# Performance work log

Measured on AMD Instinct MI355X. Metric: run time of the kernel, lower is better.

The kernel has to match this reference:

```python
import jax, jax.numpy as jnp
import numpy as np

N = 100000   # nodes
E = 1600000  # edges
C = 128      # d_model
F = 6        # LIFT_FEATURES
L = 2        # num_gcn_layers
EPS = 1e-5

def _gelu(v):
    return jax.nn.gelu(v, approximate=False)  # torch nn.GELU() default = exact erf

def setup_inputs() -> dict:
    key = jax.random.key(0)
    ks = jax.random.split(key, 24)
    def w(k, shape):
        fan_in = shape[-2] if len(shape) >= 2 else shape[-1]
        return (jax.random.normal(k, shape, jnp.float32) / np.sqrt(fan_in)).astype(jnp.float32)
    inp = {
        "x": jax.random.normal(ks[0], (1, N, 9), jnp.float32),
        "edge_index": jax.random.randint(ks[1], (2, E), 0, N, jnp.int32),
        "edge_values": jax.random.uniform(ks[2], (E,), jnp.float32),
        # lift MLP
        "lift_w1": w(ks[3], (F, C)), "lift_b1": jnp.zeros((C,), jnp.float32),
        "lift_w2": w(ks[4], (C, C)), "lift_b2": jnp.zeros((C,), jnp.float32),
        # GCN layer params stacked over L layers
        "self_w": w(ks[5], (L, C, C)),  "self_b": jnp.zeros((L, C), jnp.float32),
        "neigh_w": w(ks[6], (L, C, C)), "neigh_b": jnp.zeros((L, C), jnp.float32),
        "gate_w1": w(ks[7], (L, 2 * C, C)), "gate_b1": jnp.zeros((L, C), jnp.float32),
        "gate_w2": w(ks[8], (L, C, C)),     "gate_b2": jnp.zeros((L, C), jnp.float32),
        # final LayerNorm
        "norm_g": jnp.ones((C,), jnp.float32), "norm_b": jnp.zeros((C,), jnp.float32),
    }
    return inp

def reference(x, edge_index, edge_values,
              lift_w1, lift_b1, lift_w2, lift_b2,
              self_w, self_b, neigh_w, neigh_b,
              gate_w1, gate_b1, gate_w2, gate_b2,
              norm_g, norm_b):
    # node_feats = x[..., 3:], B == 1 path -> work on [N, F]
    nf = x[0, :, 3:]
    h = _gelu(nf @ lift_w1 + lift_b1) @ lift_w2 + lift_b2  # [N, C]
    row, col = edge_index[0], edge_index[1]
    for l in range(L):
        neighbor = h @ neigh_w[l] + neigh_b[l]                 # [N, C]
        messages = neighbor[col] * edge_values[:, None]        # gather + weight [E, C]
        aggr = jnp.zeros_like(h).at[row].add(messages)         # scatter-add [N, C]
        self_f = h @ self_w[l] + self_b[l]                     # [N, C]
        u = jnp.concatenate([self_f, aggr], axis=-1)           # [N, 2C]
        u = _gelu(u @ gate_w1[l] + gate_b1[l]) @ gate_w2[l] + gate_b2[l]
        h = h + u
    mu = jnp.mean(h, axis=-1, keepdims=True)
    var = jnp.mean(jnp.square(h - mu), axis=-1, keepdims=True)
    h = (h - mu) * jax.lax.rsqrt(var + EPS) * norm_g + norm_b
    return h[None]  # [1, N, C]
```

## Files before the change

kernel.cpp:

```cpp
#include <hip/hip_runtime.h>
#include <math.h>

#define C 128

typedef unsigned short u16;
typedef __attribute__((ext_vector_type(8))) short short8;
typedef __attribute__((ext_vector_type(4))) float f32x4;

__device__ __forceinline__ float gelu_f(float v) {
    return 0.5f * v * (1.0f + erff(v * 0.70710678118654752f));
}

__device__ __forceinline__ u16 f2bf(float f) {
    unsigned u = __float_as_uint(f);
    unsigned r = (u + 0x7fffu + ((u >> 16) & 1u)) >> 16;
    return (u16)r;
}
__device__ __forceinline__ float b2f(u16 u) {
    return __uint_as_float(((unsigned)u) << 16);
}

__device__ __forceinline__ void g2lds16(const void* g, void* l) {
    __builtin_amdgcn_global_load_lds(
        (const __attribute__((address_space(1))) unsigned int*)g,
        (__attribute__((address_space(3))) unsigned int*)l, 16, 0, 0);
}

__global__ void prep_weights_kernel(const float* __restrict__ self_w,
                                    const float* __restrict__ self_b,
                                    const float* __restrict__ neigh_w,
                                    const float* __restrict__ neigh_b,
                                    const float* __restrict__ gate_w1,
                                    const float* __restrict__ gate_b1,
                                    float* __restrict__ Wc, float* __restrict__ bc,
                                    float* __restrict__ Wn1, float* __restrict__ bv,
                                    int L_) {
    const int y = blockIdx.y;
    const int i = blockIdx.x;
    const int j = threadIdx.x;
    if (y < L_) {
        const int l = y;
        const float* gw = gate_w1 + (size_t)l * 256 * C;
        if (i < C) {
            const float* swr = self_w + (size_t)l * C * C + (size_t)i * C;
            float s = 0.f;
            for (int k = 0; k < C; ++k) s += swr[k] * gw[k * C + j];
            Wc[(size_t)l * C * C + (size_t)i * C + j] = s;
        } else {
            const float* sbr = self_b + (size_t)l * C;
            float s = gate_b1[(size_t)l * C + j];
            for (int k = 0; k < C; ++k) s += sbr[k] * gw[k * C + j];
            bc[(size_t)l * C + j] = s;
        }
    } else {
        const int l = y - L_;
        const float* gw = gate_w1 + (size_t)l * 256 * C + (size_t)C * C;
        if (i < C) {
            const float* nwr = neigh_w + (size_t)l * C * C + (size_t)i * C;
            float s = 0.f;
            for (int k = 0; k < C; ++k) s += nwr[k] * gw[k * C + j];
            Wn1[(size_t)l * C * C + (size_t)i * C + j] = s;
        } else {
            const float* nbr = neigh_b + (size_t)l * C;
            float s = 0.f;
            for (int k = 0; k < C; ++k) s += nbr[k] * gw[k * C + j];
            bv[(size_t)l * C + j] = s;
        }
    }
}

__global__ void wsplit_kernel(const float* __restrict__ lw2, const float* __restrict__ gw2,
                              const float* __restrict__ Wc, const float* __restrict__ Wn1,
                              u16* __restrict__ wh, u16* __restrict__ wl) {
    const int col = blockIdx.x;
    const int mat = blockIdx.y;
    const int k = threadIdx.x;
    const float* src;
    if (mat == 0)      src = lw2;
    else if (mat <= 2) src = gw2 + (size_t)(mat - 1) * 16384;
    else if (mat <= 4) src = Wc + (size_t)(mat - 3) * 16384;
    else               src = Wn1 + (size_t)(mat - 5) * 16384;
    float v = src[k * C + col];
    u16 hi = f2bf(v);
    size_t di = (size_t)mat * 16384 + (size_t)col * C + k;
    wh[di] = hi;
    wl[di] = f2bf(v - b2f(hi));
}

__global__ void lift_hidden_kernel(const float* __restrict__ x,
                                   const float* __restrict__ w1,
                                   const float* __restrict__ b1,
                                   u16* __restrict__ oh, u16* __restrict__ ol, int N) {
    int idx = blockIdx.x * 256 + threadIdx.x;
    if (idx >= N * C) return;
    int n = idx >> 7, c = idx & 127;
    const float* xr = x + n * 9 + 3;
    float s = b1[c];
#pragma unroll
    for (int f = 0; f < 6; ++f) s += xr[f] * w1[f * C + c];
    s = gelu_f(s);
    u16 hi = f2bf(s);
    oh[idx] = hi;
    ol[idx] = f2bf(s - b2f(hi));
}

__global__ __launch_bounds__(256, 2)
void gemm_mfma_kernel(const u16* __restrict__ A0h, const u16* __restrict__ A0l,
                      const u16* __restrict__ W0h, const u16* __restrict__ W0l,
                      const u16* __restrict__ A1h, const u16* __restrict__ A1l,
                      const u16* __restrict__ W1h, const u16* __restrict__ W1l,
                      const float* __restrict__ bias,
                      const float* __restrict__ bias2,
                      const float* __restrict__ rowscale,
                      const u16* __restrict__ Rh, const u16* __restrict__ Rl,
                      u16* __restrict__ Oh, u16* __restrict__ Ol,
                      const float* __restrict__ lng, const float* __restrict__ lnb,
                      float* __restrict__ outF,
                      int M, int nsrc, int act) {
    __shared__ __align__(16) char smem[128 * 132 * 4];
    u16* lds0 = (u16*)smem;
    const int t = threadIdx.x;
    const int l = t & 63;
    const int w = t >> 6;
    const int wr = w >> 1, wc = w & 1;
    const int m0 = blockIdx.x * 128;
    const int kg = l >> 4;
    const int swz = l & 7;
    const int l15 = l & 15;

    f32x4 acc[4][4];
#pragma unroll
    for (int m = 0; m < 4; ++m)
#pragma unroll
        for (int n = 0; n < 4; ++n) acc[m][n] = (f32x4)(0.f);

    for (int sidx = 0; sidx < nsrc; ++sidx) {
        const u16* Ah = sidx ? A1h : A0h;
        const u16* Al = sidx ? A1l : A0l;
        const u16* Wh = sidx ? W1h : W0h;
        const u16* Wl = sidx ? W1l : W0l;
        for (int kh = 0; kh < 2; ++kh) {
            const u16* gp[4] = {Ah, Al, Wh, Wl};
#pragma unroll
            for (int p = 0; p < 4; ++p) {
#pragma unroll
                for (int it = 0; it < 4; ++it) {
                    int chunk = it * 256 + t;
                    int row = chunk >> 3;
                    int cl = (chunk & 7) ^ (row & 7);
                    int grow = (p < 2) ? ((m0 + row < M) ? m0 + row : M - 1) : row;
                    const u16* src = gp[p] + (size_t)grow * C + kh * 64 + cl * 8;
                    g2lds16(src, lds0 + (size_t)p * 8192 + chunk * 8);
                }
            }
            __syncthreads();
#pragma unroll
            for (int s = 0; s < 2; ++s) {
                const int ci = ((s * 4 + kg) ^ swz) * 16;
                short8 ah[4], al[4], bh[4], bl[4];
#pragma unroll
                for (int m = 0; m < 4; ++m) {
                    int ro = (wr * 64 + m * 16 + l15) * 128;
                    ah[m] = *(const short8*)((const char*)lds0 + ro + ci);
                    al[m] = *(const short8*)((const char*)lds0 + 16384 + ro + ci);
                }
#pragma unroll
                for (int n = 0; n < 4; ++n) {
                    int ro = (wc * 64 + n * 16 + l15) * 128;
                    bh[n] = *(const short8*)((const char*)lds0 + 32768 + ro + ci);
                    bl[n] = *(const short8*)((const char*)lds0 + 49152 + ro + ci);
                }
#pragma unroll
                for (int m = 0; m < 4; ++m)
#pragma unroll
                    for (int n = 0; n < 4; ++n)
                        acc[m][n] = __builtin_amdgcn_mfma_f32_16x16x32_bf16(ah[m], bh[n], acc[m][n], 0, 0, 0);
#pragma unroll
                for (int m = 0; m < 4; ++m)
#pragma unroll
                    for (int n = 0; n < 4; ++n)
                        acc[m][n] = __builtin_amdgcn_mfma_f32_16x16x32_bf16(al[m], bh[n], acc[m][n], 0, 0, 0);
#pragma unroll
                for (int m = 0; m < 4; ++m)
#pragma unroll
                    for (int n = 0; n < 4; ++n)
                        acc[m][n] = __builtin_amdgcn_mfma_f32_16x16x32_bf16(ah[m], bl[n], acc[m][n], 0, 0, 0);
            }
            __syncthreads();
        }
    }

    float* lnt = (float*)smem;
    float bj[4], b2j[4];
#pragma unroll
    for (int n = 0; n < 4; ++n) {
        bj[n] = bias[wc * 64 + n * 16 + l15];
        b2j[n] = bias2 ? bias2[wc * 64 + n * 16 + l15] : 0.f;
    }
#pragma unroll
    for (int m = 0; m < 4; ++m) {
#pragma unroll
        for (int r = 0; r < 4; ++r) {
            int rowl = wr * 64 + m * 16 + kg * 4 + r;
            int grow = m0 + rowl;
            bool ok = grow < M;
            float rs_ = (bias2 && ok) ? rowscale[grow] : 0.f;
#pragma unroll
            for (int n = 0; n < 4; ++n) {
                int col = wc * 64 + n * 16 + l15;
                float o = acc[m][n][r] + bj[n];
                if (bias2) o += rs_ * b2j[n];
                if (act) o = gelu_f(o);
                size_t idx = (size_t)grow * C + col;
                if (Rh && ok) o += b2f(Rh[idx]) + b2f(Rl[idx]);
                if (outF) {
                    lnt[rowl * 132 + col] = o;
                } else if (ok) {
                    u16 hi = f2bf(o);
                    Oh[idx] = hi;
                    Ol[idx] = f2bf(o - b2f(hi));
                }
            }
        }
    }

    if (outF) {
        __syncthreads();
        float2 gg = *(const float2*)&lng[l << 1];
        float2 bb = *(const float2*)&lnb[l << 1];
        for (int r = 0; r < 32; ++r) {
            int rowl = w * 32 + r;
            int grow = m0 + rowl;
            if (grow >= M) break;
            float2 v = *(const float2*)&lnt[rowl * 132 + (l << 1)];
            float s = v.x + v.y;
#pragma unroll
            for (int mk = 1; mk < 64; mk <<= 1) s += __shfl_xor(s, mk, 64);
            float mu = s * (1.f / 128.f);
            float dx = v.x - mu, dy = v.y - mu;
            float q = dx * dx + dy * dy;
#pragma unroll
            for (int mk = 1; mk < 64; mk <<= 1) q += __shfl_xor(q, mk, 64);
            float rsq = 1.f / sqrtf(q * (1.f / 128.f) + 1e-5f);
            float2 o;
            o.x = dx * rsq * gg.x + bb.x;
            o.y = dy * rsq * gg.y + bb.y;
            *(float2*)&outF[(size_t)grow * C + (l << 1)] = o;
        }
    }
}

__global__ void zero_i32_kernel(int* __restrict__ p, int n) {
    int i = blockIdx.x * 256 + threadIdx.x;
    if (i < n) p[i] = 0;
}

__global__ void deg_count_kernel(const int* __restrict__ row, int* __restrict__ deg, int E) {
    int e = blockIdx.x * 256 + threadIdx.x;
    if (e < E) atomicAdd(&deg[row[e]], 1);
}

__global__ void scan_chunk_kernel(const int* __restrict__ deg, int* __restrict__ offs,
                                  int* __restrict__ part, int N) {
    __shared__ int ts[256];
    const int t = threadIdx.x;
    const int base = blockIdx.x * 1024 + t * 4;
    int v0 = (base + 0 < N) ? deg[base + 0] : 0;
    int v1 = (base + 1 < N) ? deg[base + 1] : 0;
    int v2 = (base + 2 < N) ? deg[base + 2] : 0;
    int v3 = (base + 3 < N) ? deg[base + 3] : 0;
    int l0 = v0, l1 = l0 + v1, l2 = l1 + v2, l3 = l2 + v3;
    ts[t] = l3;
    __syncthreads();
    for (int d = 1; d < 256; d <<= 1) {
        int add = (t >= d) ? ts[t - d] : 0;
        __syncthreads();
        ts[t] += add;
        __syncthreads();
    }
    int tex = ts[t] - l3;
    if (base + 0 < N) offs[base + 1] = tex + l0;
    if (base + 1 < N) offs[base + 2] = tex + l1;
    if (base + 2 < N) offs[base + 3] = tex + l2;
    if (base + 3 < N) offs[base + 4] = tex + l3;
    if (t == 255) part[blockIdx.x] = ts[255];
}

__global__ void scan_partials_kernel(int* __restrict__ part, int n) {
    __shared__ int s[128];
    const int t = threadIdx.x;
    int v = (t < n) ? part[t] : 0;
    s[t] = v;
    __syncthreads();
    for (int d = 1; d < 128; d <<= 1) {
        int add = (t >= d) ? s[t - d] : 0;
        __syncthreads();
        s[t] += add;
        __syncthreads();
    }
    if (t < n) part[t] = s[t] - v;
}

__global__ void scan_add_kernel(int* __restrict__ offs, const int* __restrict__ part,
                                int* __restrict__ cursor, int N) {
    const int t = threadIdx.x;
    const int base = blockIdx.x * 1024 + t * 4;
    const int add = part[blockIdx.x];
#pragma unroll
    for (int j = 0; j < 4; ++j) {
        int i = base + j;
        if (i < N) {
            int v = offs[i + 1] + add;
            offs[i + 1] = v;
            if (i + 1 < N) cursor[i + 1] = v;
        }
    }
    if (blockIdx.x == 0 && t == 0) {
        offs[0] = 0;
        cursor[0] = 0;
    }
}

__global__ void fill_kernel(const int* __restrict__ row, const int* __restrict__ col,
                            const float* __restrict__ ev, int* __restrict__ cursor,
                            int2* __restrict__ epack, int E) {
    int e = blockIdx.x * 256 + threadIdx.x;
    if (e >= E) return;
    int r = row[e];
    int pos = atomicAdd(&cursor[r], 1);
    int2 p;
    p.x = col[e];
    p.y = __float_as_int(ev[e]);
    epack[pos] = p;
}

__global__ __launch_bounds__(256)
void aggregate_kernel(const u16* __restrict__ nh, const u16* __restrict__ nl,
                      const int* __restrict__ offs, const int2* __restrict__ epack,
                      u16* __restrict__ oh, u16* __restrict__ ol,
                      float* __restrict__ sumev, int N) {
    const int lane = threadIdx.x & 63;
    const int node = (blockIdx.x << 2) + (threadIdx.x >> 6);
    if (node >= N) return;
    const int s = offs[node], e = offs[node + 1];
    const int ch = lane << 1;
    float ax = 0.f, ay = 0.f, bx = 0.f, by = 0.f, ssum = 0.f;
    int i = s;
    for (; i + 2 <= e; i += 2) {
        int2 p0 = epack[i];
        int2 p1 = epack[i + 1];
        float v0 = __int_as_float(p0.y);
        float v1 = __int_as_float(p1.y);
        ushort2 h0 = *(const ushort2*)&nh[(size_t)p0.x * C + ch];
        ushort2 l0 = *(const ushort2*)&nl[(size_t)p0.x * C + ch];
        ushort2 h1 = *(const ushort2*)&nh[(size_t)p1.x * C + ch];
        ushort2 l1 = *(const ushort2*)&nl[(size_t)p1.x * C + ch];
        ax += v0 * (b2f(h0.x) + b2f(l0.x));
        ay += v0 * (b2f(h0.y) + b2f(l0.y));
        bx += v1 * (b2f(h1.x) + b2f(l1.x));
        by += v1 * (b2f(h1.y) + b2f(l1.y));
        ssum += v0 + v1;
    }
    if (i < e) {
        int2 p = epack[i];
        float v = __int_as_float(p.y);
        ushort2 h0 = *(const ushort2*)&nh[(size_t)p.x * C + ch];
        ushort2 l0 = *(const ushort2*)&nl[(size_t)p.x * C + ch];
        ax += v * (b2f(h0.x) + b2f(l0.x));
        ay += v * (b2f(h0.y) + b2f(l0.y));
        ssum += v;
    }
    float sx = ax + bx, sy = ay + by;
    ushort2 ho, lo;
    ho.x = f2bf(sx); ho.y = f2bf(sy);
    lo.x = f2bf(sx - b2f(ho.x)); lo.y = f2bf(sy - b2f(ho.y));
    size_t idx = (size_t)node * C + ch;
    *(ushort2*)&oh[idx] = ho;
    *(ushort2*)&ol[idx] = lo;
    if (lane == 0) sumev[node] = ssum;
}

extern "C" void kernel_launch(void* const* d_in, const int* in_sizes, int n_in,
                              void* d_out, int out_size, void* d_ws, size_t ws_size,
                              hipStream_t stream) {
    const float* x    = (const float*)d_in[0];
    const int*   ei   = (const int*)d_in[1];
    const float* ev   = (const float*)d_in[2];
    const float* lw1  = (const float*)d_in[3];
    const float* lb1  = (const float*)d_in[4];
    const float* lw2  = (const float*)d_in[5];
    const float* lb2  = (const float*)d_in[6];
    const float* sw   = (const float*)d_in[7];
    const float* sb   = (const float*)d_in[8];
    const float* nw   = (const float*)d_in[9];
    const float* nbi  = (const float*)d_in[10];
    const float* gw1  = (const float*)d_in[11];
    const float* gb1  = (const float*)d_in[12];
    const float* gw2  = (const float*)d_in[13];
    const float* gb2  = (const float*)d_in[14];
    const float* ng   = (const float*)d_in[15];
    const float* nbt  = (const float*)d_in[16];

    const int N = in_sizes[0] / 9;
    const int E = in_sizes[2];
    const int L = in_sizes[7] / (C * C);
    const int* row = ei;
    const int* col = ei + E;

    float* out = (float*)d_out;

    char* p = (char*)d_ws;
    u16* Hh = (u16*)p; p += (size_t)N * C * 2;
    u16* Hl = (u16*)p; p += (size_t)N * C * 2;
    u16* Bh = (u16*)p; p += (size_t)N * C * 2;
    u16* Bl = (u16*)p; p += (size_t)N * C * 2;
    u16* Ch = (u16*)p; p += (size_t)N * C * 2;
    u16* Cl = (u16*)p; p += (size_t)N * C * 2;
    int2* epack = (int2*)p; p += (size_t)E * sizeof(int2);
    float* Wc  = (float*)p; p += (size_t)L * C * C * sizeof(float);
    float* Wn1 = (float*)p; p += (size_t)L * C * C * sizeof(float);
    float* bc  = (float*)p; p += (size_t)L * C * sizeof(float);
    float* bv  = (float*)p; p += (size_t)L * C * sizeof(float);
    float* sumev = (float*)p; p += (size_t)N * sizeof(float);
    u16* wh = (u16*)p; p += (size_t)7 * C * C * 2;
    u16* wl = (u16*)p; p += (size_t)7 * C * C * 2;
    int* deg    = (int*)p; p += (size_t)N * sizeof(int);
    int* offs   = (int*)p; p += (size_t)(N + 1) * sizeof(int);
    int* cursor = (int*)p; p += (size_t)N * sizeof(int);
    int* part   = (int*)p; p += 1024 * sizeof(int);

    const int NB_SCAN = (N + 1023) / 1024;
    const int GB_NODE = (N + 3) / 4;
    const int GB_EDGE = (E + 255) / 256;
    const int GB_GEMM = (N + 127) / 128;

    prep_weights_kernel<<<dim3(C + 1, 2 * L), C, 0, stream>>>(
        sw, sb, nw, nbi, gw1, gb1, Wc, bc, Wn1, bv, L);
    wsplit_kernel<<<dim3(C, 7), C, 0, stream>>>(lw2, gw2, Wc, Wn1, wh, wl);

    lift_hidden_kernel<<<(N * C + 255) / 256, 256, 0, stream>>>(x, lw1, lb1, Bh, Bl, N);
    gemm_mfma_kernel<<<GB_GEMM, 256, 0, stream>>>(
        Bh, Bl, wh, wl, nullptr, nullptr, nullptr, nullptr,
        lb2, nullptr, nullptr, nullptr, nullptr, Hh, Hl,
        nullptr, nullptr, nullptr, N, 1, 0);

    zero_i32_kernel<<<(N + 255) / 256, 256, 0, stream>>>(deg, N);
    deg_count_kernel<<<GB_EDGE, 256, 0, stream>>>(row, deg, E);
    scan_chunk_kernel<<<NB_SCAN, 256, 0, stream>>>(deg, offs, part, N);
    scan_partials_kernel<<<1, 128, 0, stream>>>(part, NB_SCAN);
    scan_add_kernel<<<NB_SCAN, 256, 0, stream>>>(offs, part, cursor, N);
    fill_kernel<<<GB_EDGE, 256, 0, stream>>>(row, col, ev, cursor, epack, E);

    for (int l = 0; l < L; ++l) {
        const u16* g2h = wh + (size_t)(1 + l) * 16384;
        const u16* g2l = wl + (size_t)(1 + l) * 16384;
        const u16* wch = wh + (size_t)(3 + l) * 16384;
        const u16* wcl = wl + (size_t)(3 + l) * 16384;
        const u16* n1h = wh + (size_t)(5 + l) * 16384;
        const u16* n1l = wl + (size_t)(5 + l) * 16384;
        const bool last = (l == L - 1);

        aggregate_kernel<<<GB_NODE, 256, 0, stream>>>(Hh, Hl, offs, epack, Ch, Cl, sumev, N);
        gemm_mfma_kernel<<<GB_GEMM, 256, 0, stream>>>(
            Hh, Hl, wch, wcl, Ch, Cl, n1h, n1l,
            bc + (size_t)l * C, bv + (size_t)l * C, sumev,
            nullptr, nullptr, Bh, Bl,
            nullptr, nullptr, nullptr, N, 2, 1);
        gemm_mfma_kernel<<<GB_GEMM, 256, 0, stream>>>(
            Bh, Bl, g2h, g2l, nullptr, nullptr, nullptr, nullptr,
            gb2 + (size_t)l * C, nullptr, nullptr,
            Hh, Hl,
            last ? nullptr : Hh, last ? nullptr : Hl,
            last ? ng : nullptr, last ? nbt : nullptr, last ? out : nullptr,
            N, 1, 0);
    }
}
```

Measured before the change: 870.2 us.

## Fuse gate GEMMs into one layer kernel and unroll aggregation by four

Merges the concat GEMM with GELU and the second gate GEMM into one kernel. The GELU intermediate is written straight into LDS as hi/lo bf16 planes instead of round-tripping through global memory, and the residual add and LayerNorm epilogue are kept. The aggregation loop is unrolled to four edges with separate accumulators, which adds memory-level parallelism on the gathers. The fused kernel keeps a larger accumulator set live, so register pressure and occupancy could suffer.

```diff
diff --git a/kernel.cpp b/kernel.cpp
--- a/kernel.cpp
+++ b/kernel.cpp
@@ -104,21 +104,26 @@
     ol[idx] = f2bf(s - b2f(hi));
 }
 
+__device__ __forceinline__ void stage_plane(const u16* __restrict__ g, char* lds_base,
+                                            int p, int t, int kh, int m0, int M,
+                                            bool clampA) {
+#pragma unroll
+    for (int it = 0; it < 4; ++it) {
+        int chunk = it * 256 + t;
+        int row = chunk >> 3;
+        int cl = (chunk & 7) ^ (row & 7);
+        int grow = clampA ? ((m0 + row < M) ? m0 + row : M - 1) : row;
+        const u16* src = g + (size_t)grow * C + kh * 64 + cl * 8;
+        g2lds16(src, lds_base + (size_t)p * 16384 + chunk * 16);
+    }
+}
+
 __global__ __launch_bounds__(256, 2)
-void gemm_mfma_kernel(const u16* __restrict__ A0h, const u16* __restrict__ A0l,
-                      const u16* __restrict__ W0h, const u16* __restrict__ W0l,
-                      const u16* __restrict__ A1h, const u16* __restrict__ A1l,
-                      const u16* __restrict__ W1h, const u16* __restrict__ W1l,
+void gemm_mfma_kernel(const u16* __restrict__ Ah_, const u16* __restrict__ Al_,
+                      const u16* __restrict__ Wh_, const u16* __restrict__ Wl_,
                       const float* __restrict__ bias,
-                      const float* __restrict__ bias2,
-                      const float* __restrict__ rowscale,
-                      const u16* __restrict__ Rh, const u16* __restrict__ Rl,
-                      u16* __restrict__ Oh, u16* __restrict__ Ol,
-                      const float* __restrict__ lng, const float* __restrict__ lnb,
-                      float* __restrict__ outF,
-                      int M, int nsrc, int act) {
-    __shared__ __align__(16) char smem[128 * 132 * 4];
-    u16* lds0 = (u16*)smem;
+                      u16* __restrict__ Oh, u16* __restrict__ Ol, int M) {
+    __shared__ __align__(16) char smem[65536];
     const int t = threadIdx.x;
     const int l = t & 63;
     const int w = t >> 6;
@@ -134,25 +139,108 @@
 #pragma unroll
         for (int n = 0; n < 4; ++n) acc[m][n] = (f32x4)(0.f);
 
-    for (int sidx = 0; sidx < nsrc; ++sidx) {
-        const u16* Ah = sidx ? A1h : A0h;
-        const u16* Al = sidx ? A1l : A0l;
-        const u16* Wh = sidx ? W1h : W0h;
-        const u16* Wl = sidx ? W1l : W0l;
+    for (int kh = 0; kh < 2; ++kh) {
+        stage_plane(Ah_, smem, 0, t, kh, m0, M, true);
+        stage_plane(Al_, smem, 1, t, kh, m0, M, true);
+        stage_plane(Wh_, smem, 2, t, kh, m0, M, false);
+        stage_plane(Wl_, smem, 3, t, kh, m0, M, false);
+        __syncthreads();
+#pragma unroll
+        for (int s = 0; s < 2; ++s) {
+            const int ci = ((s * 4 + kg) ^ swz) * 16;
+            short8 ah[4], al[4], bh[4], bl[4];
+#pragma unroll
+            for (int m = 0; m < 4; ++m) {
+                int ro = (wr * 64 + m * 16 + l15) * 128;
+                ah[m] = *(const short8*)(smem + ro + ci);
+                al[m] = *(const short8*)(smem + 16384 + ro + ci);
+            }
+#pragma unroll
+            for (int n = 0; n < 4; ++n) {
+                int ro = (wc * 64 + n * 16 + l15) * 128;
+                bh[n] = *(const short8*)(smem + 32768 + ro + ci);
+                bl[n] = *(const short8*)(smem + 49152 + ro + ci);
+            }
+#pragma unroll
+            for (int m = 0; m < 4; ++m)
+#pragma unroll
+                for (int n = 0; n < 4; ++n)
+                    acc[m][n] = __builtin_amdgcn_mfma_f32_16x16x32_bf16(ah[m], bh[n], acc[m][n], 0, 0, 0);
+#pragma unroll
+            for (int m = 0; m < 4; ++m)
+#pragma unroll
+                for (int n = 0; n < 4; ++n)
+                    acc[m][n] = __builtin_amdgcn_mfma_f32_16x16x32_bf16(al[m], bh[n], acc[m][n], 0, 0, 0);
+#pragma unroll
+            for (int m = 0; m < 4; ++m)
+#pragma unroll
+                for (int n = 0; n < 4; ++n)
+                    acc[m][n] = __builtin_amdgcn_mfma_f32_16x16x32_bf16(ah[m], bl[n], acc[m][n], 0, 0, 0);
+        }
+        __syncthreads();
+    }
+
+    float bj[4];
+#pragma unroll
+    for (int n = 0; n < 4; ++n) bj[n] = bias[wc * 64 + n * 16 + l15];
+#pragma unroll
+    for (int m = 0; m < 4; ++m)
+#pragma unroll
+        for (int r = 0; r < 4; ++r) {
+            int grow = m0 + wr * 64 + m * 16 + kg * 4 + r;
+            if (grow < M) {
+#pragma unroll
+                for (int n = 0; n < 4; ++n) {
+                    int col = wc * 64 + n * 16 + l15;
+                    float o = acc[m][n][r] + bj[n];
+                    size_t idx = (size_t)grow * C + col;
+                    u16 hi = f2bf(o);
+                    Oh[idx] = hi;
+                    Ol[idx] = f2bf(o - b2f(hi));
+                }
+            }
+        }
+}
+
+__global__ __launch_bounds__(256, 2)
+void fused_layer_kernel(const u16* __restrict__ Hh, const u16* __restrict__ Hl,
+                        const u16* __restrict__ Chh, const u16* __restrict__ Cll,
+                        const u16* __restrict__ wch, const u16* __restrict__ wcl,
+                        const u16* __restrict__ n1h, const u16* __restrict__ n1l,
+                        const u16* __restrict__ g2h, const u16* __restrict__ g2l,
+                        const float* __restrict__ bc, const float* __restrict__ bv,
+                        const float* __restrict__ sumev,
+                        const float* __restrict__ gb2,
+                        u16* __restrict__ OHh, u16* __restrict__ OHl,
+                        const float* __restrict__ lng, const float* __restrict__ lnb,
+                        float* __restrict__ outF,
+                        int M) {
+    __shared__ __align__(16) char smem[128 * 132 * 4];
+    const int t = threadIdx.x;
+    const int l = t & 63;
+    const int w = t >> 6;
+    const int wr = w >> 1, wc = w & 1;
+    const int m0 = blockIdx.x * 128;
+    const int kg = l >> 4;
+    const int swz = l & 7;
+    const int l15 = l & 15;
+
+    f32x4 acc[4][4];
+#pragma unroll
+    for (int m = 0; m < 4; ++m)
+#pragma unroll
+        for (int n = 0; n < 4; ++n) acc[m][n] = (f32x4)(0.f);
+
+    for (int sidx = 0; sidx < 2; ++sidx) {
+        const u16* Ah_ = sidx ? Chh : Hh;
+        const u16* Al_ = sidx ? Cll : Hl;
+        const u16* Wh_ = sidx ? n1h : wch;
+        const u16* Wl_ = sidx ? n1l : wcl;
         for (int kh = 0; kh < 2; ++kh) {
-            const u16* gp[4] = {Ah, Al, Wh, Wl};
-#pragma unroll
-            for (int p = 0; p < 4; ++p) {
-#pragma unroll
-                for (int it = 0; it < 4; ++it) {
-                    int chunk = it * 256 + t;
-                    int row = chunk >> 3;
-                    int cl = (chunk & 7) ^ (row & 7);
-                    int grow = (p < 2) ? ((m0 + row < M) ? m0 + row : M - 1) : row;
-                    const u16* src = gp[p] + (size_t)grow * C + kh * 64 + cl * 8;
-                    g2lds16(src, lds0 + (size_t)p * 8192 + chunk * 8);
-                }
-            }
+            stage_plane(Ah_, smem, 0, t, kh, m0, M, true);
+            stage_plane(Al_, smem, 1, t, kh, m0, M, true);
+            stage_plane(Wh_, smem, 2, t, kh, m0, M, false);
+            stage_plane(Wl_, smem, 3, t, kh, m0, M, false);
             __syncthreads();
 #pragma unroll
             for (int s = 0; s < 2; ++s) {
@@ -161,14 +249,14 @@
 #pragma unroll
                 for (int m = 0; m < 4; ++m) {
                     int ro = (wr * 64 + m * 16 + l15) * 128;
-                    ah[m] = *(const short8*)((const char*)lds0 + ro + ci);
-                    al[m] = *(const short8*)((const char*)lds0 + 16384 + ro + ci);
+                    ah[m] = *(const short8*)(smem + ro + ci);
+                    al[m] = *(const short8*)(smem + 16384 + ro + ci);
                 }
 #pragma unroll
                 for (int n = 0; n < 4; ++n) {
                     int ro = (wc * 64 + n * 16 + l15) * 128;
-                    bh[n] = *(const short8*)((const char*)lds0 + 32768 + ro + ci);
-                    bl[n] = *(const short8*)((const char*)lds0 + 49152 + ro + ci);
+                    bh[n] = *(const short8*)(smem + 32768 + ro + ci);
+                    bl[n] = *(const short8*)(smem + 49152 + ro + ci);
                 }
 #pragma unroll
                 for (int m = 0; m < 4; ++m)
@@ -190,39 +278,114 @@
         }
     }
 
+    {
+        float bj[4], b2j[4];
+#pragma unroll
+        for (int n = 0; n < 4; ++n) {
+            bj[n] = bc[wc * 64 + n * 16 + l15];
+            b2j[n] = bv[wc * 64 + n * 16 + l15];
+        }
+#pragma unroll
+        for (int m = 0; m < 4; ++m)
+#pragma unroll
+            for (int r = 0; r < 4; ++r) {
+                int grow = m0 + wr * 64 + m * 16 + kg * 4 + r;
+                float rs_ = (grow < M) ? sumev[grow] : 0.f;
+#pragma unroll
+                for (int n = 0; n < 4; ++n)
+                    acc[m][n][r] = gelu_f(acc[m][n][r] + bj[n] + rs_ * b2j[n]);
+            }
+    }
+
+    f32x4 acc2[4][4];
+#pragma unroll
+    for (int m = 0; m < 4; ++m)
+#pragma unroll
+        for (int n = 0; n < 4; ++n) acc2[m][n] = (f32x4)(0.f);
+
+    for (int kh = 0; kh < 2; ++kh) {
+        if (wc == kh) {
+#pragma unroll
+            for (int m = 0; m < 4; ++m)
+#pragma unroll
+                for (int r = 0; r < 4; ++r) {
+                    int rowl = wr * 64 + m * 16 + kg * 4 + r;
+                    int rb = rowl * 128;
+#pragma unroll
+                    for (int n = 0; n < 4; ++n) {
+                        int colk = n * 16 + l15;
+                        int pb = ((colk >> 3) ^ (rowl & 7)) * 16 + (colk & 7) * 2;
+                        float v = acc[m][n][r];
+                        u16 hi = f2bf(v);
+                        *(u16*)(smem + rb + pb) = hi;
+                        *(u16*)(smem + 16384 + rb + pb) = f2bf(v - b2f(hi));
+                    }
+                }
+        }
+        stage_plane(g2h, smem, 2, t, kh, m0, M, false);
+        stage_plane(g2l, smem, 3, t, kh, m0, M, false);
+        __syncthreads();
+#pragma unroll
+        for (int s = 0; s < 2; ++s) {
+            const int ci = ((s * 4 + kg) ^ swz) * 16;
+            short8 ah[4], al[4], bh[4], bl[4];
+#pragma unroll
+            for (int m = 0; m < 4; ++m) {
+                int ro = (wr * 64 + m * 16 + l15) * 128;
+                ah[m] = *(const short8*)(smem + ro + ci);
+                al[m] = *(const short8*)(smem + 16384 + ro + ci);
+            }
+#pragma unroll
+            for (int n = 0; n < 4; ++n) {
+                int ro = (wc * 64 + n * 16 + l15) * 128;
+                bh[n] = *(const short8*)(smem + 32768 + ro + ci);
+                bl[n] = *(const short8*)(smem + 49152 + ro + ci);
+            }
+#pragma unroll
+            for (int m = 0; m < 4; ++m)
+#pragma unroll
+                for (int n = 0; n < 4; ++n)
+                    acc2[m][n] = __builtin_amdgcn_mfma_f32_16x16x32_bf16(ah[m], bh[n], acc2[m][n], 0, 0, 0);
+#pragma unroll
+            for (int m = 0; m < 4; ++m)
+#pragma unroll
+                for (int n = 0; n < 4; ++n)
+                    acc2[m][n] = __builtin_amdgcn_mfma_f32_16x16x32_bf16(al[m], bh[n], acc2[m][n], 0, 0, 0);
+#pragma unroll
+            for (int m = 0; m < 4; ++m)
+#pragma unroll
+                for (int n = 0; n < 4; ++n)
+                    acc2[m][n] = __builtin_amdgcn_mfma_f32_16x16x32_bf16(ah[m], bl[n], acc2[m][n], 0, 0, 0);
+        }
+        __syncthreads();
+    }
+
     float* lnt = (float*)smem;
-    float bj[4], b2j[4];
-#pragma unroll
-    for (int n = 0; n < 4; ++n) {
-        bj[n] = bias[wc * 64 + n * 16 + l15];
-        b2j[n] = bias2 ? bias2[wc * 64 + n * 16 + l15] : 0.f;
-    }
-#pragma unroll
-    for (int m = 0; m < 4; ++m) {
+    float bj2[4];
+#pragma unroll
+    for (int n = 0; n < 4; ++n) bj2[n] = gb2[wc * 64 + n * 16 + l15];
+#pragma unroll
+    for (int m = 0; m < 4; ++m)
 #pragma unroll
         for (int r = 0; r < 4; ++r) {
             int rowl = wr * 64 + m * 16 + kg * 4 + r;
             int grow = m0 + rowl;
             bool ok = grow < M;
-            float rs_ = (bias2 && ok) ? rowscale[grow] : 0.f;
 #pragma unroll
             for (int n = 0; n < 4; ++n) {
                 int col = wc * 64 + n * 16 + l15;
-                float o = acc[m][n][r] + bj[n];
-                if (bias2) o += rs_ * b2j[n];
-                if (act) o = gelu_f(o);
                 size_t idx = (size_t)grow * C + col;
-                if (Rh && ok) o += b2f(Rh[idx]) + b2f(Rl[idx]);
+                float o = acc2[m][n][r] + bj2[n];
+                if (ok) o += b2f(Hh[idx]) + b2f(Hl[idx]);
                 if (outF) {
                     lnt[rowl * 132 + col] = o;
                 } else if (ok) {
                     u16 hi = f2bf(o);
-                    Oh[idx] = hi;
-                    Ol[idx] = f2bf(o - b2f(hi));
+                    OHh[idx] = hi;
+                    OHl[idx] = f2bf(o - b2f(hi));
                 }
             }
         }
-    }
 
     if (outF) {
         __syncthreads();
@@ -344,33 +507,42 @@
     if (node >= N) return;
     const int s = offs[node], e = offs[node + 1];
     const int ch = lane << 1;
-    float ax = 0.f, ay = 0.f, bx = 0.f, by = 0.f, ssum = 0.f;
+    float a0x = 0.f, a0y = 0.f, a1x = 0.f, a1y = 0.f;
+    float a2x = 0.f, a2y = 0.f, a3x = 0.f, a3y = 0.f;
+    float ssum = 0.f;
     int i = s;
-    for (; i + 2 <= e; i += 2) {
+    for (; i + 4 <= e; i += 4) {
         int2 p0 = epack[i];
         int2 p1 = epack[i + 1];
-        float v0 = __int_as_float(p0.y);
-        float v1 = __int_as_float(p1.y);
+        int2 p2 = epack[i + 2];
+        int2 p3 = epack[i + 3];
+        float v0 = __int_as_float(p0.y), v1 = __int_as_float(p1.y);
+        float v2 = __int_as_float(p2.y), v3 = __int_as_float(p3.y);
         ushort2 h0 = *(const ushort2*)&nh[(size_t)p0.x * C + ch];
-        ushort2 l0 = *(const ushort2*)&nl[(size_t)p0.x * C + ch];
         ushort2 h1 = *(const ushort2*)&nh[(size_t)p1.x * C + ch];
-        ushort2 l1 = *(const ushort2*)&nl[(size_t)p1.x * C + ch];
-        ax += v0 * (b2f(h0.x) + b2f(l0.x));
-        ay += v0 * (b2f(h0.y) + b2f(l0.y));
-        bx += v1 * (b2f(h1.x) + b2f(l1.x));
-        by += v1 * (b2f(h1.y) + b2f(l1.y));
-        ssum += v0 + v1;
-    }
-    if (i < e) {
+        ushort2 h2 = *(const ushort2*)&nh[(size_t)p2.x * C + ch];
+        ushort2 h3 = *(const ushort2*)&nh[(size_t)p3.x * C + ch];
+        ushort2 q0 = *(const ushort2*)&nl[(size_t)p0.x * C + ch];
+        ushort2 q1 = *(const ushort2*)&nl[(size_t)p1.x * C + ch];
+        ushort2 q2 = *(const ushort2*)&nl[(size_t)p2.x * C + ch];
+        ushort2 q3 = *(const ushort2*)&nl[(size_t)p3.x * C + ch];
+        a0x += v0 * (b2f(h0.x) + b2f(q0.x)); a0y += v0 * (b2f(h0.y) + b2f(q0.y));
+        a1x += v1 * (b2f(h1.x) + b2f(q1.x)); a1y += v1 * (b2f(h1.y) + b2f(q1.y));
+        a2x += v2 * (b2f(h2.x) + b2f(q2.x)); a2y += v2 * (b2f(h2.y) + b2f(q2.y));
+        a3x += v3 * (b2f(h3.x) + b2f(q3.x)); a3y += v3 * (b2f(h3.y) + b2f(q3.y));
+        ssum += (v0 + v1) + (v2 + v3);
+    }
+    for (; i < e; ++i) {
         int2 p = epack[i];
         float v = __int_as_float(p.y);
         ushort2 h0 = *(const ushort2*)&nh[(size_t)p.x * C + ch];
-        ushort2 l0 = *(const ushort2*)&nl[(size_t)p.x * C + ch];
-        ax += v * (b2f(h0.x) + b2f(l0.x));
-        ay += v * (b2f(h0.y) + b2f(l0.y));
+        ushort2 q0 = *(const ushort2*)&nl[(size_t)p.x * C + ch];
+        a0x += v * (b2f(h0.x) + b2f(q0.x));
+        a0y += v * (b2f(h0.y) + b2f(q0.y));
         ssum += v;
     }
-    float sx = ax + bx, sy = ay + by;
+    float sx = (a0x + a1x) + (a2x + a3x);
+    float sy = (a0y + a1y) + (a2y + a3y);
     ushort2 ho, lo;
     ho.x = f2bf(sx); ho.y = f2bf(sy);
     lo.x = f2bf(sx - b2f(ho.x)); lo.y = f2bf(sy - b2f(ho.y));
@@ -439,10 +611,7 @@
     wsplit_kernel<<<dim3(C, 7), C, 0, stream>>>(lw2, gw2, Wc, Wn1, wh, wl);
 
     lift_hidden_kernel<<<(N * C + 255) / 256, 256, 0, stream>>>(x, lw1, lb1, Bh, Bl, N);
-    gemm_mfma_kernel<<<GB_GEMM, 256, 0, stream>>>(
-        Bh, Bl, wh, wl, nullptr, nullptr, nullptr, nullptr,
-        lb2, nullptr, nullptr, nullptr, nullptr, Hh, Hl,
-        nullptr, nullptr, nullptr, N, 1, 0);
+    gemm_mfma_kernel<<<GB_GEMM, 256, 0, stream>>>(Bh, Bl, wh, wl, lb2, Hh, Hl, N);
 
     zero_i32_kernel<<<(N + 255) / 256, 256, 0, stream>>>(deg, N);
     deg_count_kernel<<<GB_EDGE, 256, 0, stream>>>(row, deg, E);
@@ -461,17 +630,12 @@
         const bool last = (l == L - 1);
 
         aggregate_kernel<<<GB_NODE, 256, 0, stream>>>(Hh, Hl, offs, epack, Ch, Cl, sumev, N);
-        gemm_mfma_kernel<<<GB_GEMM, 256, 0, stream>>>(
-            Hh, Hl, wch, wcl, Ch, Cl, n1h, n1l,
+        fused_layer_kernel<<<GB_GEMM, 256, 0, stream>>>(
+            Hh, Hl, Ch, Cl, wch, wcl, n1h, n1l, g2h, g2l,
             bc + (size_t)l * C, bv + (size_t)l * C, sumev,
-            nullptr, nullptr, Bh, Bl,
-            nullptr, nullptr, nullptr, N, 2, 1);
-        gemm_mfma_kernel<<<GB_GEMM, 256, 0, stream>>>(
-            Bh, Bl, g2h, g2l, nullptr, nullptr, nullptr, nullptr,
-            gb2 + (size_t)l * C, nullptr, nullptr,
+            gb2 + (size_t)l * C,
             Hh, Hl,
-            last ? nullptr : Hh, last ? nullptr : Hl,
             last ? ng : nullptr, last ? nbt : nullptr, last ? out : nullptr,
-            N, 1, 0);
-    }
-}
+            N);
+    }
+}
```

Measured after the change: 926.1 us. 6.4% more time.

## Load GEMM MFMA operands directly from global memory and unroll aggregation by four

Applied to the files above, without the earlier changes.

The GEMM kernel no longer stages A and W tiles through LDS with global_load_lds and barriers. Each lane now reads its MFMA fragments straight from global memory, relying on cache for reuse, and the launch bound rises to 3 blocks per SM. The LayerNorm epilogue is rewritten to reduce sum and sum-of-squares across lanes with shuffles and a small LDS exchange, in place of a full 128x132 float tile. The aggregate kernel unrolls the edge loop by four with independent accumulators to get more gathers in flight. Direct global fragment loads are uncoalesced, duplicate reads across waves, and the one-pass variance formula is slightly less numerically robust.

```diff
diff --git a/kernel.cpp b/kernel.cpp
--- a/kernel.cpp
+++ b/kernel.cpp
@@ -18,12 +18,6 @@
 }
 __device__ __forceinline__ float b2f(u16 u) {
     return __uint_as_float(((unsigned)u) << 16);
-}
-
-__device__ __forceinline__ void g2lds16(const void* g, void* l) {
-    __builtin_amdgcn_global_load_lds(
-        (const __attribute__((address_space(1))) unsigned int*)g,
-        (__attribute__((address_space(3))) unsigned int*)l, 16, 0, 0);
 }
 
 __global__ void prep_weights_kernel(const float* __restrict__ self_w,
@@ -104,29 +98,41 @@
     ol[idx] = f2bf(s - b2f(hi));
 }
 
-__global__ __launch_bounds__(256, 2)
-void gemm_mfma_kernel(const u16* __restrict__ A0h, const u16* __restrict__ A0l,
-                      const u16* __restrict__ W0h, const u16* __restrict__ W0l,
-                      const u16* __restrict__ A1h, const u16* __restrict__ A1l,
-                      const u16* __restrict__ W1h, const u16* __restrict__ W1l,
-                      const float* __restrict__ bias,
-                      const float* __restrict__ bias2,
-                      const float* __restrict__ rowscale,
-                      const u16* __restrict__ Rh, const u16* __restrict__ Rl,
-                      u16* __restrict__ Oh, u16* __restrict__ Ol,
-                      const float* __restrict__ lng, const float* __restrict__ lnb,
-                      float* __restrict__ outF,
-                      int M, int nsrc, int act) {
-    __shared__ __align__(16) char smem[128 * 132 * 4];
-    u16* lds0 = (u16*)smem;
+__global__ __launch_bounds__(256, 3)
+void gemm_direct_kernel(const u16* __restrict__ A0h, const u16* __restrict__ A0l,
+                        const u16* __restrict__ W0h, const u16* __restrict__ W0l,
+                        const u16* __restrict__ A1h, const u16* __restrict__ A1l,
+                        const u16* __restrict__ W1h, const u16* __restrict__ W1l,
+                        const float* __restrict__ bias,
+                        const float* __restrict__ bias2,
+                        const float* __restrict__ rowscale,
+                        const u16* __restrict__ Rh, const u16* __restrict__ Rl,
+                        u16* __restrict__ Oh, u16* __restrict__ Ol,
+                        const float* __restrict__ lng, const float* __restrict__ lnb,
+                        float* __restrict__ outF,
+                        int M, int nsrc, int act) {
+    __shared__ float2 ldsS[128][2];
     const int t = threadIdx.x;
-    const int l = t & 63;
+    const int lane = t & 63;
     const int w = t >> 6;
     const int wr = w >> 1, wc = w & 1;
     const int m0 = blockIdx.x * 128;
-    const int kg = l >> 4;
-    const int swz = l & 7;
-    const int l15 = l & 15;
+    const int kg = lane >> 4;
+    const int l15 = lane & 15;
+    const int kgo = kg * 8;
+
+    int aOff[4], wOff[4];
+#pragma unroll
+    for (int m = 0; m < 4; ++m) {
+        int grow = m0 + wr * 64 + m * 16 + l15;
+        if (grow >= M) grow = M - 1;
+        aOff[m] = grow * C + kgo;
+    }
+#pragma unroll
+    for (int n = 0; n < 4; ++n) {
+        int col = wc * 64 + n * 16 + l15;
+        wOff[n] = col * C + kgo;
+    }
 
     f32x4 acc[4][4];
 #pragma unroll
@@ -139,58 +145,38 @@
         const u16* Al = sidx ? A1l : A0l;
         const u16* Wh = sidx ? W1h : W0h;
         const u16* Wl = sidx ? W1l : W0l;
-        for (int kh = 0; kh < 2; ++kh) {
-            const u16* gp[4] = {Ah, Al, Wh, Wl};
-#pragma unroll
-            for (int p = 0; p < 4; ++p) {
-#pragma unroll
-                for (int it = 0; it < 4; ++it) {
-                    int chunk = it * 256 + t;
-                    int row = chunk >> 3;
-                    int cl = (chunk & 7) ^ (row & 7);
-                    int grow = (p < 2) ? ((m0 + row < M) ? m0 + row : M - 1) : row;
-                    const u16* src = gp[p] + (size_t)grow * C + kh * 64 + cl * 8;
-                    g2lds16(src, lds0 + (size_t)p * 8192 + chunk * 8);
-                }
+#pragma unroll
+        for (int ks = 0; ks < 4; ++ks) {
+            const int ko = ks * 32;
+            short8 ah[4], al[4], bh[4], bl[4];
+#pragma unroll
+            for (int m = 0; m < 4; ++m) {
+                ah[m] = *(const short8*)(Ah + aOff[m] + ko);
+                al[m] = *(const short8*)(Al + aOff[m] + ko);
             }
-            __syncthreads();
-#pragma unroll
-            for (int s = 0; s < 2; ++s) {
-                const int ci = ((s * 4 + kg) ^ swz) * 16;
-                short8 ah[4], al[4], bh[4], bl[4];
-#pragma unroll
-                for (int m = 0; m < 4; ++m) {
-                    int ro = (wr * 64 + m * 16 + l15) * 128;
-                    ah[m] = *(const short8*)((const char*)lds0 + ro + ci);
-                    al[m] = *(const short8*)((const char*)lds0 + 16384 + ro + ci);
-                }
-#pragma unroll
-                for (int n = 0; n < 4; ++n) {
-                    int ro = (wc * 64 + n * 16 + l15) * 128;
-                    bh[n] = *(const short8*)((const char*)lds0 + 32768 + ro + ci);
-                    bl[n] = *(const short8*)((const char*)lds0 + 49152 + ro + ci);
-                }
-#pragma unroll
-                for (int m = 0; m < 4; ++m)
-#pragma unroll
-                    for (int n = 0; n < 4; ++n)
-                        acc[m][n] = __builtin_amdgcn_mfma_f32_16x16x32_bf16(ah[m], bh[n], acc[m][n], 0, 0, 0);
-#pragma unroll
-                for (int m = 0; m < 4; ++m)
-#pragma unroll
-                    for (int n = 0; n < 4; ++n)
-                        acc[m][n] = __builtin_amdgcn_mfma_f32_16x16x32_bf16(al[m], bh[n], acc[m][n], 0, 0, 0);
-#pragma unroll
-                for (int m = 0; m < 4; ++m)
-#pragma unroll
-                    for (int n = 0; n < 4; ++n)
-                        acc[m][n] = __builtin_amdgcn_mfma_f32_16x16x32_bf16(ah[m], bl[n], acc[m][n], 0, 0, 0);
+#pragma unroll
+            for (int n = 0; n < 4; ++n) {
+                bh[n] = *(const short8*)(Wh + wOff[n] + ko);
+                bl[n] = *(const short8*)(Wl + wOff[n] + ko);
             }
-            __syncthreads();
+#pragma unroll
+            for (int m = 0; m < 4; ++m)
+#pragma unroll
+                for (int n = 0; n < 4; ++n)
+                    acc[m][n] = __builtin_amdgcn_mfma_f32_16x16x32_bf16(ah[m], bh[n], acc[m][n], 0, 0, 0);
+#pragma unroll
+            for (int m = 0; m < 4; ++m)
+#pragma unroll
+                for (int n = 0; n < 4; ++n)
+                    acc[m][n] = __builtin_amdgcn_mfma_f32_16x16x32_bf16(al[m], bh[n], acc[m][n], 0, 0, 0);
+#pragma unroll
+            for (int m = 0; m < 4; ++m)
+#pragma unroll
+                for (int n = 0; n < 4; ++n)
+                    acc[m][n] = __builtin_amdgcn_mfma_f32_16x16x32_bf16(ah[m], bl[n], acc[m][n], 0, 0, 0);
         }
     }
 
-    float* lnt = (float*)smem;
     float bj[4], b2j[4];
 #pragma unroll
     for (int n = 0; n < 4; ++n) {
@@ -198,55 +184,91 @@
         b2j[n] = bias2 ? bias2[wc * 64 + n * 16 + l15] : 0.f;
     }
 #pragma unroll
-    for (int m = 0; m < 4; ++m) {
+    for (int m = 0; m < 4; ++m)
 #pragma unroll
         for (int r = 0; r < 4; ++r) {
-            int rowl = wr * 64 + m * 16 + kg * 4 + r;
-            int grow = m0 + rowl;
-            bool ok = grow < M;
-            float rs_ = (bias2 && ok) ? rowscale[grow] : 0.f;
+            int grow = m0 + wr * 64 + m * 16 + kg * 4 + r;
+            float rs_ = (bias2 && grow < M) ? rowscale[grow] : 0.f;
 #pragma unroll
             for (int n = 0; n < 4; ++n) {
-                int col = wc * 64 + n * 16 + l15;
-                float o = acc[m][n][r] + bj[n];
-                if (bias2) o += rs_ * b2j[n];
+                float o = acc[m][n][r] + bj[n] + rs_ * b2j[n];
                 if (act) o = gelu_f(o);
-                size_t idx = (size_t)grow * C + col;
-                if (Rh && ok) o += b2f(Rh[idx]) + b2f(Rl[idx]);
-                if (outF) {
-                    lnt[rowl * 132 + col] = o;
-                } else if (ok) {
-                    u16 hi = f2bf(o);
-                    Oh[idx] = hi;
-                    Ol[idx] = f2bf(o - b2f(hi));
+                acc[m][n][r] = o;
+            }
+        }
+
+    if (!outF) {
+#pragma unroll
+        for (int m = 0; m < 4; ++m)
+#pragma unroll
+            for (int r = 0; r < 4; ++r) {
+                int grow = m0 + wr * 64 + m * 16 + kg * 4 + r;
+                if (grow < M) {
+#pragma unroll
+                    for (int n = 0; n < 4; ++n) {
+                        int col = wc * 64 + n * 16 + l15;
+                        size_t idx = (size_t)grow * C + col;
+                        float o = acc[m][n][r];
+                        if (Rh) o += b2f(Rh[idx]) + b2f(Rl[idx]);
+                        u16 hi = f2bf(o);
+                        Oh[idx] = hi;
+                        Ol[idx] = f2bf(o - b2f(hi));
+                    }
                 }
             }
+    } else {
+#pragma unroll
+        for (int m = 0; m < 4; ++m)
+#pragma unroll
+            for (int r = 0; r < 4; ++r) {
+                int rowl = wr * 64 + m * 16 + kg * 4 + r;
+                int grow = m0 + rowl;
+                bool ok = grow < M;
+                float s1 = 0.f, s2 = 0.f;
+#pragma unroll
+                for (int n = 0; n < 4; ++n) {
+                    int col = wc * 64 + n * 16 + l15;
+                    size_t idx = (size_t)grow * C + col;
+                    float o = acc[m][n][r];
+                    if (ok && Rh) o += b2f(Rh[idx]) + b2f(Rl[idx]);
+                    acc[m][n][r] = o;
+                    s1 += o;
+                    s2 += o * o;
+                }
+#pragma unroll
+                for (int mk = 1; mk < 16; mk <<= 1) {
+                    s1 += __shfl_xor(s1, mk, 64);
+                    s2 += __shfl_xor(s2, mk, 64);
+                }
+                if (l15 == 0) ldsS[rowl][wc] = make_float2(s1, s2);
+            }
+        __syncthreads();
+        float gj[4], bbj[4];
+#pragma unroll
+        for (int n = 0; n < 4; ++n) {
+            gj[n] = lng[wc * 64 + n * 16 + l15];
+            bbj[n] = lnb[wc * 64 + n * 16 + l15];
         }
-    }
-
-    if (outF) {
-        __syncthreads();
-        float2 gg = *(const float2*)&lng[l << 1];
-        float2 bb = *(const float2*)&lnb[l << 1];
-        for (int r = 0; r < 32; ++r) {
-            int rowl = w * 32 + r;
-            int grow = m0 + rowl;
-            if (grow >= M) break;
-            float2 v = *(const float2*)&lnt[rowl * 132 + (l << 1)];
-            float s = v.x + v.y;
-#pragma unroll
-            for (int mk = 1; mk < 64; mk <<= 1) s += __shfl_xor(s, mk, 64);
-            float mu = s * (1.f / 128.f);
-            float dx = v.x - mu, dy = v.y - mu;
-            float q = dx * dx + dy * dy;
-#pragma unroll
-            for (int mk = 1; mk < 64; mk <<= 1) q += __shfl_xor(q, mk, 64);
-            float rsq = 1.f / sqrtf(q * (1.f / 128.f) + 1e-5f);
-            float2 o;
-            o.x = dx * rsq * gg.x + bb.x;
-            o.y = dy * rsq * gg.y + bb.y;
-            *(float2*)&outF[(size_t)grow * C + (l << 1)] = o;
-        }
+#pragma unroll
+        for (int m = 0; m < 4; ++m)
+#pragma unroll
+            for (int r = 0; r < 4; ++r) {
+                int rowl = wr * 64 + m * 16 + kg * 4 + r;
+                int grow = m0 + rowl;
+                float2 pa = ldsS[rowl][0];
+                float2 pb = ldsS[rowl][1];
+                float mu = (pa.x + pb.x) * (1.f / 128.f);
+                float var = (pa.y + pb.y) * (1.f / 128.f) - mu * mu;
+                float rsq = 1.f / sqrtf(var + 1e-5f);
+                if (grow < M) {
+#pragma unroll
+                    for (int n = 0; n < 4; ++n) {
+                        int col = wc * 64 + n * 16 + l15;
+                        outF[(size_t)grow * C + col] =
+                            (acc[m][n][r] - mu) * rsq * gj[n] + bbj[n];
+                    }
+                }
+            }
     }
 }
 
@@ -344,33 +366,42 @@
     if (node >= N) return;
     const int s = offs[node], e = offs[node + 1];
     const int ch = lane << 1;
-    float ax = 0.f, ay = 0.f, bx = 0.f, by = 0.f, ssum = 0.f;
+    float a0x = 0.f, a0y = 0.f, a1x = 0.f, a1y = 0.f;
+    float a2x = 0.f, a2y = 0.f, a3x = 0.f, a3y = 0.f;
+    float ssum = 0.f;
     int i = s;
-    for (; i + 2 <= e; i += 2) {
+    for (; i + 4 <= e; i += 4) {
         int2 p0 = epack[i];
         int2 p1 = epack[i + 1];
-        float v0 = __int_as_float(p0.y);
-        float v1 = __int_as_float(p1.y);
+        int2 p2 = epack[i + 2];
+        int2 p3 = epack[i + 3];
+        float v0 = __int_as_float(p0.y), v1 = __int_as_float(p1.y);
+        float v2 = __int_as_float(p2.y), v3 = __int_as_float(p3.y);
         ushort2 h0 = *(const ushort2*)&nh[(size_t)p0.x * C + ch];
-        ushort2 l0 = *(const ushort2*)&nl[(size_t)p0.x * C + ch];
         ushort2 h1 = *(const ushort2*)&nh[(size_t)p1.x * C + ch];
-        ushort2 l1 = *(const ushort2*)&nl[(size_t)p1.x * C + ch];
-        ax += v0 * (b2f(h0.x) + b2f(l0.x));
-        ay += v0 * (b2f(h0.y) + b2f(l0.y));
-        bx += v1 * (b2f(h1.x) + b2f(l1.x));
-        by += v1 * (b2f(h1.y) + b2f(l1.y));
-        ssum += v0 + v1;
-    }
-    if (i < e) {
+        ushort2 h2 = *(const ushort2*)&nh[(size_t)p2.x * C + ch];
+        ushort2 h3 = *(const ushort2*)&nh[(size_t)p3.x * C + ch];
+        ushort2 q0 = *(const ushort2*)&nl[(size_t)p0.x * C + ch];
+        ushort2 q1 = *(const ushort2*)&nl[(size_t)p1.x * C + ch];
+        ushort2 q2 = *(const ushort2*)&nl[(size_t)p2.x * C + ch];
+        ushort2 q3 = *(const ushort2*)&nl[(size_t)p3.x * C + ch];
+        a0x += v0 * (b2f(h0.x) + b2f(q0.x)); a0y += v0 * (b2f(h0.y) + b2f(q0.y));
+        a1x += v1 * (b2f(h1.x) + b2f(q1.x)); a1y += v1 * (b2f(h1.y) + b2f(q1.y));
+        a2x += v2 * (b2f(h2.x) + b2f(q2.x)); a2y += v2 * (b2f(h2.y) + b2f(q2.y));
+        a3x += v3 * (b2f(h3.x) + b2f(q3.x)); a3y += v3 * (b2f(h3.y) + b2f(q3.y));
+        ssum += (v0 + v1) + (v2 + v3);
+    }
+    for (; i < e; ++i) {
         int2 p = epack[i];
         float v = __int_as_float(p.y);
         ushort2 h0 = *(const ushort2*)&nh[(size_t)p.x * C + ch];
-        ushort2 l0 = *(const ushort2*)&nl[(size_t)p.x * C + ch];
-        ax += v * (b2f(h0.x) + b2f(l0.x));
-        ay += v * (b2f(h0.y) + b2f(l0.y));
+        ushort2 q0 = *(const ushort2*)&nl[(size_t)p.x * C + ch];
+        a0x += v * (b2f(h0.x) + b2f(q0.x));
+        a0y += v * (b2f(h0.y) + b2f(q0.y));
         ssum += v;
     }
-    float sx = ax + bx, sy = ay + by;
+    float sx = (a0x + a1x) + (a2x + a3x);
+    float sy = (a0y + a1y) + (a2y + a3y);
     ushort2 ho, lo;
     ho.x = f2bf(sx); ho.y = f2bf(sy);
     lo.x = f2bf(sx - b2f(ho.x)); lo.y = f2bf(sy - b2f(ho.y));
@@ -439,7 +470,7 @@
     wsplit_kernel<<<dim3(C, 7), C, 0, stream>>>(lw2, gw2, Wc, Wn1, wh, wl);
 
     lift_hidden_kernel<<<(N * C + 255) / 256, 256, 0, stream>>>(x, lw1, lb1, Bh, Bl, N);
-    gemm_mfma_kernel<<<GB_GEMM, 256, 0, stream>>>(
+    gemm_direct_kernel<<<GB_GEMM, 256, 0, stream>>>(
         Bh, Bl, wh, wl, nullptr, nullptr, nullptr, nullptr,
         lb2, nullptr, nullptr, nullptr, nullptr, Hh, Hl,
         nullptr, nullptr, nullptr, N, 1, 0);
@@ -461,12 +492,12 @@
         const bool last = (l == L - 1);
 
         aggregate_kernel<<<GB_NODE, 256, 0, stream>>>(Hh, Hl, offs, epack, Ch, Cl, sumev, N);
-        gemm_mfma_kernel<<<GB_GEMM, 256, 0, stream>>>(
+        gemm_direct_kernel<<<GB_GEMM, 256, 0, stream>>>(
             Hh, Hl, wch, wcl, Ch, Cl, n1h, n1l,
             bc + (size_t)l * C, bv + (size_t)l * C, sumev,
             nullptr, nullptr, Bh, Bl,
             nullptr, nullptr, nullptr, N, 2, 1);
-        gemm_mfma_kernel<<<GB_GEMM, 256, 0, stream>>>(
+        gemm_direct_kernel<<<GB_GEMM, 256, 0, stream>>>(
             Bh, Bl, g2h, g2l, nullptr, nullptr, nullptr, nullptr,
             gb2 + (size_t)l * C, nullptr, nullptr,
             Hh, Hl,
```

Measured after the change: 1.327 ms. +52.5%, slower.
